# Kernel tuning notes

Hardware: AMD Instinct MI355X
Metric: run time of the kernel (lower is better)

The kernel has to match this reference:

```python
import jax, jax.numpy as jnp
import numpy as np

N, S, C = 2048, 14, 30  # batch, grid, channels (B=2 boxes*5 + 20 classes)
L_COORD, L_NOOBJ = 5.0, 0.5


def setup_inputs() -> dict:
    key = jax.random.key(0)
    k1, k2, k3 = jax.random.split(key, 3)
    pred = jax.random.uniform(k1, (N, S, S, C), minval=0.05, maxval=1.0, dtype=jnp.float32)
    target = jax.random.uniform(k2, (N, S, S, C), minval=0.05, maxval=1.0, dtype=jnp.float32)
    conf = (jax.random.uniform(k3, (N, S, S)) > 0.7).astype(jnp.float32)
    target = target.at[..., 4].set(conf)
    return {"pred": pred, "target": target}


def _to_xyxy(b):
    # b[..., :2] = center (grid units, divided by 14), b[..., 2:4] = w,h (image units)
    xy = b[..., :2] / 14.0
    wh = b[..., 2:4]
    return jnp.concatenate([xy - 0.5 * wh, xy + 0.5 * wh], axis=-1)


def _yolo_loss(pred, target):
    n = pred.shape[0]
    coo = (target[..., 4] > 0).astype(pred.dtype)   # [N,S,S] object mask
    noo = 1.0 - coo                                  # no-object mask
    pb = pred[..., :10].reshape(pred.shape[:3] + (2, 5))    # [N,S,S,2,5]
    tb = target[..., :10].reshape(target.shape[:3] + (2, 5))

    # IoU of the 2 predicted boxes vs the FIRST target box of the cell
    p_xy = _to_xyxy(pb)              # [N,S,S,2,4]
    t_xy = _to_xyxy(tb[..., 0, :])   # [N,S,S,4]
    lt = jnp.maximum(p_xy[..., :2], t_xy[..., None, :2])
    rb = jnp.minimum(p_xy[..., 2:], t_xy[..., None, 2:])
    wh = jnp.clip(rb - lt, 0.0)
    inter = wh[..., 0] * wh[..., 1]                          # [N,S,S,2]
    a1 = (p_xy[..., 2] - p_xy[..., 0]) * (p_xy[..., 3] - p_xy[..., 1])
    a2 = ((t_xy[..., 2] - t_xy[..., 0]) * (t_xy[..., 3] - t_xy[..., 1]))[..., None]
    iou = inter / (a1 + a2 - inter)

    # responsible box = argmax IoU (selection only; IoU value never enters the
    # loss because the original writes max_iou into cols :4 but reads col 4=0)
    r = jnp.argmax(jax.lax.stop_gradient(iou), axis=-1)      # [N,S,S]
    idx = r[..., None, None]
    resp_p = jnp.take_along_axis(pb, idx, axis=3)[..., 0, :]      # [N,S,S,5]
    resp_t = jnp.take_along_axis(tb, idx, axis=3)[..., 0, :]
    nresp_p = jnp.take_along_axis(pb, 1 - idx, axis=3)[..., 0, :]

    cm = coo[..., None]
    loc = jnp.sum(cm * (resp_p[..., :2] - resp_t[..., :2]) ** 2) \
        + jnp.sum(cm * (jnp.sqrt(resp_p[..., 2:4]) - jnp.sqrt(resp_t[..., 2:4])) ** 2)
    contain = jnp.sum(coo * resp_p[..., 4] ** 2)       # target IoU col 4 is 0 in original
    not_contain = jnp.sum(coo * nresp_p[..., 4] ** 2)  # target conf zeroed in original
    noobj = jnp.sum(noo * ((pred[..., 4] - target[..., 4]) ** 2
                           + (pred[..., 9] - target[..., 9]) ** 2))
    cls = jnp.sum(cm * (pred[..., 10:] - target[..., 10:]) ** 2)
    return (L_COORD * loc + 2.0 * contain + not_contain + L_NOOBJ * noobj + cls) / n


def reference(pred, target):
    return _yolo_loss(pred, target)
```

## Files before the change

### kernel.cpp

```cpp
#include <hip/hip_runtime.h>


constexpr int N_IMG  = 2048;
constexpr int NC     = 30;
constexpr int CELLS  = N_IMG * 14 * 14;
constexpr int BLOCK  = 256;
constexpr int CPB    = 64;
constexpr int NCHT   = CELLS / CPB;
constexpr int GRID   = 768;
constexpr float INV14 = 1.0f / 14.0f;

constexpr int FPB   = 2 * CPB * NC;
constexpr int SLOTS = FPB / 4;
constexpr int SPW   = SLOTS / 4;
constexpr int PREDS = CPB * NC / 4;

__device__ __forceinline__ void gload16(const void* g, void* l) {
    __builtin_amdgcn_global_load_lds(
        (const __attribute__((address_space(1))) void*)g,
        (__attribute__((address_space(3))) void*)l, 16, 0, 0);
}

__device__ __forceinline__ float cell_loss(const float* __restrict__ cp,
                                           const float* __restrict__ ct)
{
    float pv[NC], tv[NC];
    const float2* p2 = reinterpret_cast<const float2*>(cp);
    const float2* t2 = reinterpret_cast<const float2*>(ct);
    #pragma unroll
    for (int i = 0; i < NC / 2; ++i) {
        float2 a = p2[i]; pv[2*i] = a.x; pv[2*i+1] = a.y;
        float2 b = t2[i]; tv[2*i] = b.x; tv[2*i+1] = b.y;
    }

    const float coo = (tv[4] > 0.0f) ? 1.0f : 0.0f;

    const float txc = tv[0] * INV14, tyc = tv[1] * INV14;
    const float tx1 = txc - 0.5f * tv[2], ty1 = tyc - 0.5f * tv[3];
    const float tx2 = txc + 0.5f * tv[2], ty2 = tyc + 0.5f * tv[3];
    const float t_area = (tx2 - tx1) * (ty2 - ty1);

    float i0, u0;
    {
        const float xc = pv[0] * INV14, yc = pv[1] * INV14;
        const float x1 = xc - 0.5f * pv[2], y1 = yc - 0.5f * pv[3];
        const float x2 = xc + 0.5f * pv[2], y2 = yc + 0.5f * pv[3];
        const float a1 = (x2 - x1) * (y2 - y1);
        const float wx = fmaxf(fminf(x2, tx2) - fmaxf(x1, tx1), 0.0f);
        const float wy = fmaxf(fminf(y2, ty2) - fmaxf(y1, ty1), 0.0f);
        i0 = wx * wy;
        u0 = a1 + t_area - i0;
    }
    float i1, u1;
    {
        const float xc = pv[5] * INV14, yc = pv[6] * INV14;
        const float x1 = xc - 0.5f * pv[7], y1 = yc - 0.5f * pv[8];
        const float x2 = xc + 0.5f * pv[7], y2 = yc + 0.5f * pv[8];
        const float a1 = (x2 - x1) * (y2 - y1);
        const float wx = fmaxf(fminf(x2, tx2) - fmaxf(x1, tx1), 0.0f);
        const float wy = fmaxf(fminf(y2, ty2) - fmaxf(y1, ty1), 0.0f);
        i1 = wx * wy;
        u1 = a1 + t_area - i1;
    }

    const bool sel = (i1 * u0) > (i0 * u1);
    const float rp0 = sel ? pv[5] : pv[0];
    const float rp1 = sel ? pv[6] : pv[1];
    const float rp2 = sel ? pv[7] : pv[2];
    const float rp3 = sel ? pv[8] : pv[3];
    const float rp4 = sel ? pv[9] : pv[4];
    const float rt0 = sel ? tv[5] : tv[0];
    const float rt1 = sel ? tv[6] : tv[1];
    const float rt2 = sel ? tv[7] : tv[2];
    const float rt3 = sel ? tv[8] : tv[3];
    const float nrp4 = sel ? pv[4] : pv[9];

    const float d0 = rp0 - rt0, d1 = rp1 - rt1;
    const float d2 = sqrtf(rp2) - sqrtf(rt2);
    const float d3 = sqrtf(rp3) - sqrtf(rt3);
    const float loc     = d0*d0 + d1*d1 + d2*d2 + d3*d3;
    const float contain = rp4 * rp4;
    const float notc    = nrp4 * nrp4;
    const float e4 = pv[4] - tv[4], e9 = pv[9] - tv[9];
    const float noobj = e4*e4 + e9*e9;
    float cls = 0.0f;
    #pragma unroll
    for (int c = 10; c < NC; ++c) { const float d = pv[c] - tv[c]; cls += d*d; }

    return coo * (5.0f * loc + 2.0f * contain + notc + cls)
         + (1.0f - coo) * (0.5f * noobj);
}

__global__ __launch_bounds__(BLOCK)
void yolo_main(const float* __restrict__ pred,
               const float* __restrict__ targ,
               float* __restrict__ partial)
{
    __shared__ float sbuf[3 * FPB];

    const int tid = threadIdx.x;
    const int bid = blockIdx.x;
    const int wv  = tid >> 6;
    const int ln  = tid & 63;

    auto stage = [&](float* lbuf, int chunk) {
        const size_t fbase = (size_t)chunk * (size_t)(CPB * NC);
        const int wbase = wv * SPW;
        const float4* gsrc = (wv < 2)
            ? reinterpret_cast<const float4*>(pred + fbase) + wbase
            : reinterpret_cast<const float4*>(targ + fbase) + (wbase - PREDS);
        float4* lb = reinterpret_cast<float4*>(lbuf) + wbase;
        #pragma unroll
        for (int i = 0; i < 3; ++i)
            gload16(gsrc + i * 64 + ln, lb + i * 64 + ln);
        if (ln < 48)
            gload16(gsrc + 192 + ln, lb + 192 + ln);
    };

    const int n = (NCHT - bid + GRID - 1) / GRID;

    stage(sbuf, bid);
    stage(sbuf + FPB, bid + GRID);
    asm volatile("s_waitcnt vmcnt(4)" ::: "memory");
    __builtin_amdgcn_sched_barrier(0);
    __builtin_amdgcn_s_barrier();
    __builtin_amdgcn_sched_barrier(0);

    float acc = 0.0f;
    for (int k = 0; k < n; ++k) {
        const bool pre = (k + 2 < n);
        if (pre) stage(sbuf + ((k + 2) % 3) * FPB, bid + (k + 2) * GRID);

        if (tid < CPB) {
            const float* b = sbuf + (k % 3) * FPB;
            acc += cell_loss(b + tid * NC, b + CPB * NC + tid * NC);
        }

        if (pre) asm volatile("s_waitcnt vmcnt(4)" ::: "memory");
        else     asm volatile("s_waitcnt vmcnt(0)" ::: "memory");
        __builtin_amdgcn_sched_barrier(0);
        __builtin_amdgcn_s_barrier();
        __builtin_amdgcn_sched_barrier(0);
    }

    __shared__ float wsum[BLOCK / 64];
    #pragma unroll
    for (int o = 32; o > 0; o >>= 1) acc += __shfl_down(acc, o, 64);
    if ((tid & 63) == 0) wsum[tid >> 6] = acc;
    __syncthreads();
    if (tid == 0)
        partial[bid] = wsum[0] + wsum[1] + wsum[2] + wsum[3];
}

__global__ __launch_bounds__(64)
void yolo_final(const float* __restrict__ partial, float* __restrict__ out)
{
    const int tid = threadIdx.x;
    double s = 0.0;
    #pragma unroll
    for (int i = 0; i < GRID / 64; ++i) s += (double)partial[tid + i * 64];
    #pragma unroll
    for (int o = 32; o > 0; o >>= 1) s += __shfl_down(s, o, 64);
    if (tid == 0) out[0] = (float)(s / (double)N_IMG);
}

extern "C" void kernel_launch(void* const* d_in, const int* in_sizes, int n_in,
                              void* d_out, int out_size, void* d_ws, size_t ws_size,
                              hipStream_t stream)
{
    const float* pred = (const float*)d_in[0];
    const float* targ = (const float*)d_in[1];
    float* out        = (float*)d_out;
    float* partial    = (float*)d_ws;

    yolo_main<<<GRID, BLOCK, 0, stream>>>(pred, targ, partial);
    yolo_final<<<1, 64, 0, stream>>>(partial, out);
}
```

Measured before the change: 22.67 us.

## Give each wave its own triple-buffered LDS pipeline and drop block barriers

The block-wide cooperative staging of 64 cells per chunk is replaced with per-wave private triple buffers of 32 cells, so each wave loads and computes its own chunks. This removes the s_barrier on every iteration and lets waves run independently, and it raises compute utilisation from one wave per block to half of every wave. The grid shrinks to 256 blocks with hardcoded per-wave iteration counts of 13 and 12 chunks, which adds more outstanding loads per wave but ties correctness to the exact problem size.

After: 25.39 us. 12.0% more time.

```diff
diff --git a/kernel.cpp b/kernel.cpp
--- a/kernel.cpp
+++ b/kernel.cpp
@@ -5,15 +5,15 @@
 constexpr int NC     = 30;
 constexpr int CELLS  = N_IMG * 14 * 14;
 constexpr int BLOCK  = 256;
-constexpr int CPB    = 64;
-constexpr int NCHT   = CELLS / CPB;
-constexpr int GRID   = 768;
+constexpr int CPW    = 32;
+constexpr int NCHT   = CELLS / CPW;
+constexpr int GRID   = 256;
+constexpr int WAVES  = GRID * 4;
 constexpr float INV14 = 1.0f / 14.0f;
 
-constexpr int FPB   = 2 * CPB * NC;
-constexpr int SLOTS = FPB / 4;
-constexpr int SPW   = SLOTS / 4;
-constexpr int PREDS = CPB * NC / 4;
+constexpr int FPW   = 2 * CPW * NC;
+constexpr int SLW   = FPW / 4;
+constexpr int PREDW = CPW * NC / 4;
 
 __device__ __forceinline__ void gload16(const void* g, void* l) {
     __builtin_amdgcn_global_load_lds(
@@ -96,50 +96,53 @@
                const float* __restrict__ targ,
                float* __restrict__ partial)
 {
-    __shared__ float sbuf[3 * FPB];
+    __shared__ float sbuf[4][3][FPW];
 
     const int tid = threadIdx.x;
     const int bid = blockIdx.x;
     const int wv  = tid >> 6;
     const int ln  = tid & 63;
 
-    auto stage = [&](float* lbuf, int chunk) {
-        const size_t fbase = (size_t)chunk * (size_t)(CPB * NC);
-        const int wbase = wv * SPW;
-        const float4* gsrc = (wv < 2)
-            ? reinterpret_cast<const float4*>(pred + fbase) + wbase
-            : reinterpret_cast<const float4*>(targ + fbase) + (wbase - PREDS);
-        float4* lb = reinterpret_cast<float4*>(lbuf) + wbase;
+    float* const wbase = &sbuf[wv][0][0];
+
+    auto stage = [&](int b, int chunk) {
+        const size_t fb = (size_t)chunk * (size_t)(CPW * NC);
+        const float4* gp = reinterpret_cast<const float4*>(pred + fb);
+        const float4* gt = reinterpret_cast<const float4*>(targ + fb);
+        float4* lb = reinterpret_cast<float4*>(wbase + b * FPW);
         #pragma unroll
-        for (int i = 0; i < 3; ++i)
-            gload16(gsrc + i * 64 + ln, lb + i * 64 + ln);
-        if (ln < 48)
-            gload16(gsrc + 192 + ln, lb + 192 + ln);
+        for (int i = 0; i < 7; ++i) {
+            const int s = i * 64 + ln;
+            gload16(s < PREDW ? gp + s : gt + (s - PREDW), lb + s);
+        }
+        if (ln < 32) {
+            const int s = 448 + ln;
+            gload16(gt + (s - PREDW), lb + s);
+        }
     };
 
-    const int n = (NCHT - bid + GRID - 1) / GRID;
+    const int g = bid + wv * 256;
+    const int n = (wv == 0) ? 13 : 12;
 
-    stage(sbuf, bid);
-    stage(sbuf + FPB, bid + GRID);
-    asm volatile("s_waitcnt vmcnt(4)" ::: "memory");
-    __builtin_amdgcn_sched_barrier(0);
-    __builtin_amdgcn_s_barrier();
-    __builtin_amdgcn_sched_barrier(0);
+    stage(0, g);
+    stage(1, g + WAVES);
 
     float acc = 0.0f;
     for (int k = 0; k < n; ++k) {
-        const bool pre = (k + 2 < n);
-        if (pre) stage(sbuf + ((k + 2) % 3) * FPB, bid + (k + 2) * GRID);
+        if (k + 2 < n) stage((k + 2) % 3, g + (k + 2) * WAVES);
 
-        if (tid < CPB) {
-            const float* b = sbuf + (k % 3) * FPB;
-            acc += cell_loss(b + tid * NC, b + CPB * NC + tid * NC);
+        if (k + 2 < n)
+            asm volatile("s_waitcnt vmcnt(16) lgkmcnt(0)" ::: "memory");
+        else if (k + 1 < n)
+            asm volatile("s_waitcnt vmcnt(8) lgkmcnt(0)" ::: "memory");
+        else
+            asm volatile("s_waitcnt vmcnt(0) lgkmcnt(0)" ::: "memory");
+        __builtin_amdgcn_sched_barrier(0);
+
+        if (ln < CPW) {
+            const float* b = wbase + (k % 3) * FPW;
+            acc += cell_loss(b + ln * NC, b + CPW * NC + ln * NC);
         }
-
-        if (pre) asm volatile("s_waitcnt vmcnt(4)" ::: "memory");
-        else     asm volatile("s_waitcnt vmcnt(0)" ::: "memory");
-        __builtin_amdgcn_sched_barrier(0);
-        __builtin_amdgcn_s_barrier();
         __builtin_amdgcn_sched_barrier(0);
     }
 
```
